# Kernel tuning notes

Hardware: AMD Instinct MI355X
Metric: run time of the kernel (lower is better)

The kernel has to match this reference:

```python
import jax, jax.numpy as jnp
import numpy as np

B, T, D, H, C = 256, 512, 1, 1024, 10
STD = 0.01


def setup_inputs() -> dict:
    key = jax.random.key(0)
    ks = jax.random.split(key, 14)
    n = lambda k, shape: STD * jax.random.normal(k, shape, dtype=jnp.float32)
    return {
        "x": jax.random.normal(ks[0], (B, T), dtype=jnp.float32),
        "w_gx": n(ks[1], (D, H)), "w_gh": n(ks[2], (H, H)), "b_g": jnp.zeros((H,), jnp.float32),
        "w_ix": n(ks[3], (D, H)), "w_ih": n(ks[4], (H, H)), "b_i": jnp.zeros((H,), jnp.float32),
        "w_fx": n(ks[5], (D, H)), "w_fh": n(ks[6], (H, H)), "b_f": jnp.zeros((H,), jnp.float32),
        "w_ox": n(ks[7], (D, H)), "w_oh": n(ks[8], (H, H)), "b_o": jnp.zeros((H,), jnp.float32),
        "w_ph": n(ks[9], (H, C)), "b_p": jnp.zeros((C,), jnp.float32),
    }


def _lstm_forward(x, w_gx, w_gh, b_g, w_ix, w_ih, b_i, w_fx, w_fh, b_f,
                  w_ox, w_oh, b_o, w_ph, b_p):
    h_dim = w_gh.shape[0]
    # Fuse the 4 gate weight matrices into single GEMMs per step (cuDNN-style).
    Wx = jnp.concatenate([w_gx, w_ix, w_fx, w_ox], axis=1)   # [D, 4H]
    Wh = jnp.concatenate([w_gh, w_ih, w_fh, w_oh], axis=1)   # [H, 4H]
    b = jnp.concatenate([b_g, b_i, b_f, b_o])                # [4H]

    xt = jnp.swapaxes(x[:, :, None], 0, 1)  # [T, B, D] with D==1
    batch = x.shape[0]
    h0 = jnp.zeros((batch, h_dim), x.dtype)
    c0 = jnp.zeros((batch, h_dim), x.dtype)

    def step(carry, x_t):
        h, c = carry
        z = x_t @ Wx + h @ Wh + b                 # [B, 4H]
        g = jnp.tanh(z[:, :h_dim])
        i = jax.nn.sigmoid(z[:, h_dim:2 * h_dim])
        f = jax.nn.sigmoid(z[:, 2 * h_dim:3 * h_dim])
        o = jax.nn.sigmoid(z[:, 3 * h_dim:])
        c = g * i + c * f
        h = jnp.tanh(c) * o
        return (h, c), None

    (h, _), _ = jax.lax.scan(step, (h0, c0), xt)
    return jax.nn.softmax(h @ w_ph + b_p, axis=-1)  # [B, C]


def reference(x, w_gx, w_gh, b_g, w_ix, w_ih, b_i, w_fx, w_fh, b_f,
              w_ox, w_oh, b_o, w_ph, b_p):
    return _lstm_forward(x, w_gx, w_gh, b_g, w_ix, w_ih, b_i, w_fx, w_fh, b_f,
                         w_ox, w_oh, b_o, w_ph, b_p)
```

## Files before the change

### kernel.cpp

```cpp
#include <hip/hip_runtime.h>

#define Tt  512
#define Hd  1024
#define Cc  10
#define HBHALF (256 * 1024)

typedef short bf16x8 __attribute__((ext_vector_type(8)));
typedef float f32x4 __attribute__((ext_vector_type(4)));

__device__ __forceinline__ unsigned short f2bf(float f) {
  unsigned u = __builtin_bit_cast(unsigned, f);
  u = (u + 0x7FFFu + ((u >> 16) & 1u)) >> 16;
  return (unsigned short)u;
}
__device__ __forceinline__ float bf2f(unsigned short s) {
  unsigned u = ((unsigned)s) << 16;
  return __builtin_bit_cast(float, u);
}
__device__ __forceinline__ float sigmf_(float z) { return 1.0f / (1.0f + __expf(-z)); }
__device__ __forceinline__ float tanhf_(float z) { return 1.0f - 2.0f / (__expf(2.0f * z) + 1.0f); }

__global__ __launch_bounds__(256) void lstm_prep(
    const float* __restrict__ wgh, const float* __restrict__ wih,
    const float* __restrict__ wfh, const float* __restrict__ woh,
    unsigned short* __restrict__ whT)
{
  __shared__ float tile[64][65];
  const int bid = blockIdx.x;
  const int q  = bid >> 8;
  const int ct = (bid >> 4) & 15;
  const int kt = bid & 15;
  const float* w = (q == 0) ? wgh : (q == 1) ? wih : (q == 2) ? wfh : woh;
  const int tid = threadIdx.x;
  const int tc = tid & 63, tr = tid >> 6;
  #pragma unroll
  for (int i = 0; i < 16; ++i) {
    int kk = i * 4 + tr;
    tile[kk][tc] = w[(size_t)(kt * 64 + kk) * Hd + ct * 64 + tc];
  }
  __syncthreads();
  #pragma unroll
  for (int i = 0; i < 16; ++i) {
    int cc = i * 4 + tr;
    whT[(size_t)(q * 1024 + ct * 64 + cc) * Hd + kt * 64 + tc] = f2bf(tile[tc][cc]);
  }
}

__global__ __launch_bounds__(256) void lstm_step(
    const unsigned short* __restrict__ whT,
    const float* __restrict__ x,
    const float* __restrict__ wgx, const float* __restrict__ wix,
    const float* __restrict__ wfx, const float* __restrict__ wox,
    const float* __restrict__ bg,  const float* __restrict__ bi,
    const float* __restrict__ bfp, const float* __restrict__ bo,
    const unsigned short* __restrict__ hR,
    unsigned short* __restrict__ hW,
    float* __restrict__ cbuf,
    int t)
{
  extern __shared__ char smem[];
  char*  hls  = smem;
  float* zbuf = (float*)(smem + 65536);

  const int tid = threadIdx.x;
  const int l   = tid & 63;
  const int w4  = tid >> 6;
  const int cb  = blockIdx.x & 31;
  const int rg  = blockIdx.x >> 5;
  const int r0  = rg * 32;
  const int hc0 = cb * 32;

  {
    int rbase = w4 * 8;
    #pragma unroll
    for (int i = 0; i < 16; ++i) {
      int r = rbase + (i >> 1);
      int half = i & 1;
      char* ldsb = hls + r * 2048 + half * 1024;
      int m = half * 64 + l;
      int srcc = m ^ (r & 7);
      const char* gp = (const char*)hR + (((size_t)(r0 + r) << 10) + srcc * 8) * 2;
      __builtin_amdgcn_global_load_lds(gp, ldsb, 16, 0, 0);
    }
  }
  __syncthreads();

  const int q   = w4;
  const int lc  = l & 15;
  const int kb8 = (l >> 4) * 8;
  const int roff0 = lc * 2048;
  const int roff1 = roff0 + 16 * 2048;
  const int swz   = (l & 7) << 4;
  const int kboff = (l >> 4) * 16;
  const unsigned short* wcol0 = whT + (size_t)(q * 1024 + hc0 + lc) * Hd + kb8;
  const unsigned short* wcol1 = wcol0 + (size_t)16 * Hd;

  f32x4 acc00 = {0.f,0.f,0.f,0.f};
  f32x4 acc01 = {0.f,0.f,0.f,0.f};
  f32x4 acc10 = {0.f,0.f,0.f,0.f};
  f32x4 acc11 = {0.f,0.f,0.f,0.f};
  #pragma unroll
  for (int kc = 0; kc < 32; ++kc) {
    int boff = (kc * 64 + kboff) ^ swz;
    bf16x8 a0 = *(const bf16x8*)(hls + roff0 + boff);
    bf16x8 a1 = *(const bf16x8*)(hls + roff1 + boff);
    bf16x8 b0 = *(const bf16x8*)(wcol0 + kc * 32);
    bf16x8 b1 = *(const bf16x8*)(wcol1 + kc * 32);
    acc00 = __builtin_amdgcn_mfma_f32_16x16x32_bf16(a0, b0, acc00, 0, 0, 0);
    acc01 = __builtin_amdgcn_mfma_f32_16x16x32_bf16(a0, b1, acc01, 0, 0, 0);
    acc10 = __builtin_amdgcn_mfma_f32_16x16x32_bf16(a1, b0, acc10, 0, 0, 0);
    acc11 = __builtin_amdgcn_mfma_f32_16x16x32_bf16(a1, b1, acc11, 0, 0, 0);
  }

  {
    int colz = q * 32 + lc;
    int rb = (l >> 4) * 4;
    #pragma unroll
    for (int p = 0; p < 4; ++p) {
      zbuf[(rb + p) * 128 + colz]           = acc00[p];
      zbuf[(rb + p) * 128 + colz + 16]      = acc01[p];
      zbuf[(rb + p + 16) * 128 + colz]      = acc10[p];
      zbuf[(rb + p + 16) * 128 + colz + 16] = acc11[p];
    }
  }
  __syncthreads();

  #pragma unroll
  for (int e = 0; e < 4; ++e) {
    int idx = tid + e * 256;
    int r = idx >> 5, hc = idx & 31;
    int hcol = hc0 + hc;
    float xv = x[(size_t)(r0 + r) * Tt + t];
    float zg = zbuf[r * 128 +       hc] + xv * wgx[hcol] + bg[hcol];
    float zi = zbuf[r * 128 +  32 + hc] + xv * wix[hcol] + bi[hcol];
    float zf = zbuf[r * 128 +  64 + hc] + xv * wfx[hcol] + bfp[hcol];
    float zo = zbuf[r * 128 +  96 + hc] + xv * wox[hcol] + bo[hcol];
    float G = tanhf_(zg);
    float I = sigmf_(zi);
    float F = sigmf_(zf);
    float O = sigmf_(zo);
    size_t ci = (size_t)(r0 + r) * Hd + hcol;
    float cnew = G * I + cbuf[ci] * F;
    cbuf[ci] = cnew;
    hW[ci] = f2bf(tanhf_(cnew) * O);
  }
}

__global__ __launch_bounds__(256) void lstm_final(
    const unsigned short* __restrict__ h, const float* __restrict__ wph,
    const float* __restrict__ bp, float* __restrict__ out)
{
  __shared__ float zrow[16][10];
  const int tid = threadIdx.x;
  if (tid < 160) {
    int rr = tid / 10, c = tid - rr * 10;
    int r = blockIdx.x * 16 + rr;
    float acc = bp[c];
    for (int k = 0; k < Hd; ++k) acc += bf2f(h[(size_t)r * Hd + k]) * wph[k * Cc + c];
    zrow[rr][c] = acc;
  }
  __syncthreads();
  if (tid < 16) {
    int r = blockIdx.x * 16 + tid;
    float m = -1e30f;
    #pragma unroll
    for (int cc = 0; cc < Cc; ++cc) m = fmaxf(m, zrow[tid][cc]);
    float s = 0.f;
    float ev[Cc];
    #pragma unroll
    for (int cc = 0; cc < Cc; ++cc) { ev[cc] = __expf(zrow[tid][cc] - m); s += ev[cc]; }
    float inv = 1.0f / s;
    #pragma unroll
    for (int cc = 0; cc < Cc; ++cc) out[r * Cc + cc] = ev[cc] * inv;
  }
}

extern "C" void kernel_launch(void* const* d_in, const int* in_sizes, int n_in,
                              void* d_out, int out_size, void* d_ws, size_t ws_size,
                              hipStream_t stream) {
  const float* x   = (const float*)d_in[0];
  const float* wgx = (const float*)d_in[1];
  const float* wgh = (const float*)d_in[2];
  const float* bg  = (const float*)d_in[3];
  const float* wix = (const float*)d_in[4];
  const float* wih = (const float*)d_in[5];
  const float* bi  = (const float*)d_in[6];
  const float* wfx = (const float*)d_in[7];
  const float* wfh = (const float*)d_in[8];
  const float* bfp = (const float*)d_in[9];
  const float* wox = (const float*)d_in[10];
  const float* woh = (const float*)d_in[11];
  const float* bo  = (const float*)d_in[12];
  const float* wph = (const float*)d_in[13];
  const float* bp  = (const float*)d_in[14];
  float* out = (float*)d_out;

  unsigned short* whT  = (unsigned short*)d_ws;
  unsigned short* hbuf = (unsigned short*)((char*)d_ws + (size_t)4 * 1024 * Hd * 2);
  float* cbuf = (float*)((char*)hbuf + (size_t)2 * HBHALF * 2);

  hipMemsetAsync(hbuf, 0, (size_t)HBHALF * 2, stream);
  hipMemsetAsync(cbuf, 0, (size_t)HBHALF * 4, stream);

  hipFuncSetAttribute((const void*)lstm_step,
                      hipFuncAttributeMaxDynamicSharedMemorySize, 81920);

  lstm_prep<<<1024, 256, 0, stream>>>(wgh, wih, wfh, woh, whT);

  for (int t = 0; t < Tt; ++t) {
    const unsigned short* hR = hbuf + (size_t)(t & 1) * HBHALF;
    unsigned short*       hW = hbuf + (size_t)((t + 1) & 1) * HBHALF;
    lstm_step<<<256, 256, 81920, stream>>>(whT, x, wgx, wix, wfx, wox,
                                           bg, bi, bfp, bo, hR, hW, cbuf, t);
  }

  lstm_final<<<16, 256, 0, stream>>>(hbuf , wph, bp, out);
}
```

Measured before the change: 5.736 ms.

## Double step-kernel threads to 512, split MFMA columns across 8 waves

The per-timestep LSTM kernel now runs 512 threads per block. Each of the 8 waves computes one 16-column half of a gate instead of 4 waves each handling 32 columns, which halves the MFMA chain and weight loads per wave and adds latency hiding. The x values for the block are staged once in shared memory, and the final projection reads h with 16-byte vector loads. The cost is more threads per CU, which may limit occupancy given the 80KB of LDS per block.

Result: faster. 5.592 ms (-2.5%).

```diff
diff --git a/kernel.cpp b/kernel.cpp
--- a/kernel.cpp
+++ b/kernel.cpp
@@ -46,7 +46,7 @@
   }
 }
 
-__global__ __launch_bounds__(256) void lstm_step(
+__global__ __launch_bounds__(512) void lstm_step(
     const unsigned short* __restrict__ whT,
     const float* __restrict__ x,
     const float* __restrict__ wgx, const float* __restrict__ wix,
@@ -61,19 +61,22 @@
   extern __shared__ char smem[];
   char*  hls  = smem;
   float* zbuf = (float*)(smem + 65536);
+  __shared__ float xsh[32];
 
   const int tid = threadIdx.x;
   const int l   = tid & 63;
-  const int w4  = tid >> 6;
+  const int w   = tid >> 6;
   const int cb  = blockIdx.x & 31;
   const int rg  = blockIdx.x >> 5;
   const int r0  = rg * 32;
   const int hc0 = cb * 32;
 
+  if (tid < 32) xsh[tid] = x[(size_t)(r0 + tid) * Tt + t];
+
   {
-    int rbase = w4 * 8;
-    #pragma unroll
-    for (int i = 0; i < 16; ++i) {
+    int rbase = w * 4;
+    #pragma unroll
+    for (int i = 0; i < 8; ++i) {
       int r = rbase + (i >> 1);
       int half = i & 1;
       char* ldsb = hls + r * 2048 + half * 1024;
@@ -85,52 +88,44 @@
   }
   __syncthreads();
 
-  const int q   = w4;
-  const int lc  = l & 15;
-  const int kb8 = (l >> 4) * 8;
+  const int q  = w >> 1;
+  const int lc = l & 15;
   const int roff0 = lc * 2048;
   const int roff1 = roff0 + 16 * 2048;
   const int swz   = (l & 7) << 4;
   const int kboff = (l >> 4) * 16;
-  const unsigned short* wcol0 = whT + (size_t)(q * 1024 + hc0 + lc) * Hd + kb8;
-  const unsigned short* wcol1 = wcol0 + (size_t)16 * Hd;
-
-  f32x4 acc00 = {0.f,0.f,0.f,0.f};
-  f32x4 acc01 = {0.f,0.f,0.f,0.f};
-  f32x4 acc10 = {0.f,0.f,0.f,0.f};
-  f32x4 acc11 = {0.f,0.f,0.f,0.f};
+  const unsigned short* wcol =
+      whT + (size_t)(q * 1024 + hc0 + ((w & 1) << 4) + lc) * Hd + (l >> 4) * 8;
+
+  f32x4 acc0 = {0.f,0.f,0.f,0.f};
+  f32x4 acc1 = {0.f,0.f,0.f,0.f};
   #pragma unroll
   for (int kc = 0; kc < 32; ++kc) {
     int boff = (kc * 64 + kboff) ^ swz;
     bf16x8 a0 = *(const bf16x8*)(hls + roff0 + boff);
     bf16x8 a1 = *(const bf16x8*)(hls + roff1 + boff);
-    bf16x8 b0 = *(const bf16x8*)(wcol0 + kc * 32);
-    bf16x8 b1 = *(const bf16x8*)(wcol1 + kc * 32);
-    acc00 = __builtin_amdgcn_mfma_f32_16x16x32_bf16(a0, b0, acc00, 0, 0, 0);
-    acc01 = __builtin_amdgcn_mfma_f32_16x16x32_bf16(a0, b1, acc01, 0, 0, 0);
-    acc10 = __builtin_amdgcn_mfma_f32_16x16x32_bf16(a1, b0, acc10, 0, 0, 0);
-    acc11 = __builtin_amdgcn_mfma_f32_16x16x32_bf16(a1, b1, acc11, 0, 0, 0);
+    bf16x8 b  = *(const bf16x8*)(wcol + kc * 32);
+    acc0 = __builtin_amdgcn_mfma_f32_16x16x32_bf16(a0, b, acc0, 0, 0, 0);
+    acc1 = __builtin_amdgcn_mfma_f32_16x16x32_bf16(a1, b, acc1, 0, 0, 0);
   }
 
   {
-    int colz = q * 32 + lc;
-    int rb = (l >> 4) * 4;
+    int colz  = (w << 4) + lc;
+    int rbase = (l >> 4) * 4;
     #pragma unroll
     for (int p = 0; p < 4; ++p) {
-      zbuf[(rb + p) * 128 + colz]           = acc00[p];
-      zbuf[(rb + p) * 128 + colz + 16]      = acc01[p];
-      zbuf[(rb + p + 16) * 128 + colz]      = acc10[p];
-      zbuf[(rb + p + 16) * 128 + colz + 16] = acc11[p];
+      zbuf[(rbase + p) * 128 + colz]      = acc0[p];
+      zbuf[(rbase + p + 16) * 128 + colz] = acc1[p];
     }
   }
   __syncthreads();
 
   #pragma unroll
-  for (int e = 0; e < 4; ++e) {
-    int idx = tid + e * 256;
+  for (int e = 0; e < 2; ++e) {
+    int idx = tid + e * 512;
     int r = idx >> 5, hc = idx & 31;
     int hcol = hc0 + hc;
-    float xv = x[(size_t)(r0 + r) * Tt + t];
+    float xv = xsh[r];
     float zg = zbuf[r * 128 +       hc] + xv * wgx[hcol] + bg[hcol];
     float zi = zbuf[r * 128 +  32 + hc] + xv * wix[hcol] + bi[hcol];
     float zf = zbuf[r * 128 +  64 + hc] + xv * wfx[hcol] + bfp[hcol];
@@ -156,7 +151,12 @@
     int rr = tid / 10, c = tid - rr * 10;
     int r = blockIdx.x * 16 + rr;
     float acc = bp[c];
-    for (int k = 0; k < Hd; ++k) acc += bf2f(h[(size_t)r * Hd + k]) * wph[k * Cc + c];
+    for (int k8 = 0; k8 < 128; ++k8) {
+      bf16x8 hv = *(const bf16x8*)(h + (size_t)r * Hd + k8 * 8);
+      #pragma unroll
+      for (int e = 0; e < 8; ++e)
+        acc += bf2f((unsigned short)hv[e]) * wph[(k8 * 8 + e) * Cc + c];
+    }
     zrow[rr][c] = acc;
   }
   __syncthreads();
@@ -210,7 +210,7 @@
   for (int t = 0; t < Tt; ++t) {
     const unsigned short* hR = hbuf + (size_t)(t & 1) * HBHALF;
     unsigned short*       hW = hbuf + (size_t)((t + 1) & 1) * HBHALF;
-    lstm_step<<<256, 256, 81920, stream>>>(whT, x, wgx, wix, wfx, wox,
+    lstm_step<<<256, 512, 81920, stream>>>(whT, x, wgx, wix, wfx, wox,
                                            bg, bi, bfp, bo, hR, hW, cbuf, t);
   }
 
```
